# Optimization experiments

Measured on AMD Instinct MI355X. Metric: run time of the kernel, lower is better.

Reference implementation:

```python
import jax, jax.numpy as jnp
import numpy as np

DIM = 1024
HEADS = 16
DIM_HEAD = 64
INNER = HEADS * DIM_HEAD  # 1024
SCALE = DIM ** (-0.5)  # module scales by dim**-0.5 (not dim_head)


def setup_inputs() -> dict:
    key = jax.random.key(0)
    kx, kqkv, kwo, kbo = jax.random.split(key, 4)
    x = jax.random.normal(kx, (2, 2048, DIM), dtype=jnp.float32)
    W_qkv = jax.random.normal(kqkv, (DIM, 3 * INNER), dtype=jnp.float32) * (DIM ** -0.5)
    W_out = jax.random.normal(kwo, (INNER, DIM), dtype=jnp.float32) * (INNER ** -0.5)
    b_out = jax.random.normal(kbo, (DIM,), dtype=jnp.float32) * 0.01
    return {"x": x, "W_qkv": W_qkv, "W_out": W_out, "b_out": b_out}


def reference(x, W_qkv, W_out, b_out):
    b, n, _ = x.shape
    qkv = x @ W_qkv  # [b, n, 3*inner]
    q, k, v = jnp.split(qkv, 3, axis=-1)
    # [b, n, h*d] -> [b, h, n, d]
    reshape = lambda t: t.reshape(b, n, HEADS, DIM_HEAD).transpose(0, 2, 1, 3)
    q, k, v = reshape(q), reshape(k), reshape(v)
    dots = jnp.einsum('bhid,bhjd->bhij', q, k) * SCALE  # [b, h, n, n]
    attn = jax.nn.softmax(dots, axis=-1)
    out = jnp.einsum('bhij,bhjd->bhid', attn, v)  # [b, h, n, d]
    out = out.transpose(0, 2, 1, 3).reshape(b, n, INNER)
    return out @ W_out + b_out
```

## Files before the change

### kernel.cpp

```cpp
#include <hip/hip_runtime.h>

typedef __bf16 bf16x8 __attribute__((ext_vector_type(8)));
typedef __bf16 bf16x4 __attribute__((ext_vector_type(4)));
typedef __bf16 bf16x2 __attribute__((ext_vector_type(2)));
typedef float f32x4 __attribute__((ext_vector_type(4)));
typedef float f32x16 __attribute__((ext_vector_type(16)));
typedef int i32x4 __attribute__((ext_vector_type(4)));
typedef unsigned int u32x2 __attribute__((ext_vector_type(2)));

__device__ __forceinline__ void async16(void* lds, const void* g) {
  __builtin_amdgcn_global_load_lds(
      (__attribute__((address_space(1))) unsigned int*)(g),
      (__attribute__((address_space(3))) unsigned int*)(lds), 16, 0, 0);
}

__device__ __forceinline__ unsigned int pack2(float a, float b) {
  bf16x2 t;
  t[0] = (__bf16)a;
  t[1] = (__bf16)b;
  return __builtin_bit_cast(unsigned int, t);
}

__device__ __forceinline__ void plswap(unsigned int& d, unsigned int& s) {
#if __has_builtin(__builtin_amdgcn_permlane32_swap)
  u32x2 r = __builtin_amdgcn_permlane32_swap(d, s, false, false);
  d = r[0];
  s = r[1];
#else
  asm("v_permlane32_swap_b32 %0, %1" : "+v"(d), "+v"(s));
#endif
}

__device__ __forceinline__ int detect_block(const unsigned short* win, int* cnt_sh) {
  if (threadIdx.x == 0) *cnt_sh = 0;
  __syncthreads();
  int c = 0;
#pragma unroll
  for (int j = 0; j < 8; j++) {
    const unsigned short u = win[threadIdx.x * 8 + j];
    if (((u >> 7) & 0xFF) >= 0xC0) c++;
  }
  if (c) atomicAdd(cnt_sh, c);
  __syncthreads();
  return (*cnt_sh >= 64) ? 1 : 0;
}

__global__ __launch_bounds__(256) void prep(
    const void* __restrict__ x, const void* __restrict__ Wqkv,
    const void* __restrict__ Wout, __bf16* __restrict__ xb,
    __bf16* __restrict__ WqkvT, __bf16* __restrict__ WoutT,
    int* __restrict__ flagp)
{
  __shared__ __bf16 tile[64 * 65];
  __shared__ int cnt;
  const int bx = blockIdx.x;
  const int t = threadIdx.x;

  if (bx < 2048) {
    const long base = (long)bx * 2048;
    const int f = detect_block((const unsigned short*)x + base, &cnt);
    if (bx == 0 && t == 0) *flagp = f;
    const long i = base + t * 8;
    if (f) {
      const float* s = (const float*)x;
#pragma unroll
      for (int j = 0; j < 8; j++) xb[i + j] = (__bf16)s[i + j];
    } else {
      *(bf16x8*)&xb[i] = *(const bf16x8*)((const __bf16*)x + i);
    }
    return;
  }

  const void* in;  __bf16* out;  int R = 1024, C, tcx, tr;
  if (bx < 2816) {
    const int idx = bx - 2048;
    in = Wqkv; out = WqkvT; C = 3072; tcx = (idx % 48) * 64; tr = (idx / 48) * 64;
  } else {
    const int idx = bx - 2816;
    in = Wout; out = WoutT; C = 1024; tcx = (idx % 16) * 64; tr = (idx / 16) * 64;
  }
  const int f = detect_block((const unsigned short*)in + (long)tr * C + tcx, &cnt);
#pragma unroll
  for (int i = 0; i < 16; i++) {
    const int idx = t + 256 * i;
    const int r = idx >> 6, c = idx & 63;
    const long g = (long)(tr + r) * C + tcx + c;
    tile[r * 65 + c] = f ? (__bf16)((const float*)in)[g] : ((const __bf16*)in)[g];
  }
  __syncthreads();
#pragma unroll
  for (int i = 0; i < 16; i++) {
    const int idx = t + 256 * i;
    const int r = idx >> 6, c = idx & 63;
    out[(long)(tcx + r) * R + tr + c] = tile[c * 65 + r];
  }
}

__global__ __launch_bounds__(256, 3) void gemm_qkv(
    const __bf16* __restrict__ A, const __bf16* __restrict__ Bt,
    __bf16* __restrict__ Cqk, __bf16* __restrict__ Vt)
{
  __shared__ __bf16 smem[17408];
  const int t = threadIdx.x;
  const int l = t & 63;
  const int w = t >> 6;
  const int wr = w >> 1, wc = w & 1;
  const long m0 = (long)blockIdx.x * 128;
  const long n0 = (long)blockIdx.y * 128;
  const int K = 1024;

  const int srow = w * 16 + (l >> 2);
  const int skof = (l & 3) * 8;
  const __bf16* gA = A + (m0 + srow) * (long)K + skof;
  const __bf16* gB = Bt + (n0 + srow) * (long)K + skof;
  const int Ao[2] = {0, 8192}, Bo[2] = {4096, 12288};
  const int lof = w * 512 + l * 8;

  async16(smem + Ao[0] + lof,        gA);
  async16(smem + Ao[0] + 2048 + lof, gA + 64 * (long)K);
  async16(smem + Bo[0] + lof,        gB);
  async16(smem + Bo[0] + 2048 + lof, gB + 64 * (long)K);
  gA += 32; gB += 32;
  __syncthreads();

  f32x4 acc[4][4] = {};

  for (int it = 0; it < 32; it++) {
    if (it < 31) {
      const int nb = (it + 1) & 1;
      async16(smem + Ao[nb] + lof,        gA);
      async16(smem + Ao[nb] + 2048 + lof, gA + 64 * (long)K);
      async16(smem + Bo[nb] + lof,        gB);
      async16(smem + Bo[nb] + 2048 + lof, gB + 64 * (long)K);
      gA += 32; gB += 32;
    }
    const __bf16* As = smem + Ao[it & 1];
    const __bf16* Bs = smem + Bo[it & 1];
    bf16x8 af[4], bfr[4];
#pragma unroll
    for (int mi = 0; mi < 4; mi++)
      af[mi] = *(const bf16x8*)&As[(wr * 64 + mi * 16 + (l & 15)) * 32 + (l >> 4) * 8];
#pragma unroll
    for (int ni = 0; ni < 4; ni++)
      bfr[ni] = *(const bf16x8*)&Bs[(wc * 64 + ni * 16 + (l & 15)) * 32 + (l >> 4) * 8];
#pragma unroll
    for (int mi = 0; mi < 4; mi++)
#pragma unroll
      for (int ni = 0; ni < 4; ni++)
        acc[mi][ni] = __builtin_amdgcn_mfma_f32_16x16x32_bf16(af[mi], bfr[ni], acc[mi][ni], 0, 0, 0);
    __syncthreads();
  }

  if (n0 < 2048) {
#pragma unroll
    for (int mi = 0; mi < 4; mi++)
#pragma unroll
      for (int ni = 0; ni < 4; ni++) {
        const long col = n0 + wc * 64 + ni * 16 + (l & 15);
#pragma unroll
        for (int r = 0; r < 4; r++) {
          const long row = m0 + wr * 64 + mi * 16 + (l >> 4) * 4 + r;
          Cqk[row * 2048 + col] = (__bf16)acc[mi][ni][r];
        }
      }
  } else {
#pragma unroll
    for (int mi = 0; mi < 4; mi++)
#pragma unroll
      for (int ni = 0; ni < 4; ni++) {
        const int c = wc * 64 + ni * 16 + (l & 15);
        const int r = wr * 64 + mi * 16 + (l >> 4) * 4;
        bf16x4 pk;
#pragma unroll
        for (int k = 0; k < 4; k++) pk[k] = (__bf16)acc[mi][ni][k];
        *(bf16x4*)&smem[c * 136 + r] = pk;
      }
    __syncthreads();
    const int b = (int)(m0 >> 11);
    const int nbase = (int)(m0 & 2047);
#pragma unroll
    for (int i = 0; i < 8; i++) {
      const int c = (t >> 4) + i * 16;
      const int r8 = (t & 15) * 8;
      const bf16x8 v = *(const bf16x8*)&smem[c * 136 + r8];
      const int vcol = (int)(n0 - 2048) + c;
      *(bf16x8*)&Vt[((long)(b * 16 + (vcol >> 6)) * 64 + (vcol & 63)) * 2048 + nbase + r8] = v;
    }
  }
}

__global__ __launch_bounds__(256, 2) void gemm_out(
    const __bf16* __restrict__ A, const __bf16* __restrict__ Bt,
    const void* __restrict__ bias_raw, void* __restrict__ C,
    const int* __restrict__ flagp)
{
  __shared__ __bf16 smem[12288];
  const int t = threadIdx.x;
  const int l = t & 63;
  const int w = t >> 6;
  const int wr = w >> 1, wc = w & 1;
  const long m0 = (long)blockIdx.x * 128;
  const long n0 = (long)blockIdx.y * 64;
  const int of = *flagp;
  const int K = 1024;

  const int srow = w * 16 + (l >> 2);
  const int skof = (l & 3) * 8;
  const __bf16* gA = A + (m0 + srow) * (long)K + skof;
  const __bf16* gB = Bt + (n0 + srow) * (long)K + skof;
  const int Ao[2] = {0, 6144}, Bo[2] = {4096, 10240};
  const int lof = w * 512 + l * 8;

  async16(smem + Ao[0] + lof,        gA);
  async16(smem + Ao[0] + 2048 + lof, gA + 64 * (long)K);
  async16(smem + Bo[0] + lof,        gB);
  gA += 32; gB += 32;
  __syncthreads();

  f32x4 acc[4][2] = {};

  for (int it = 0; it < 32; it++) {
    if (it < 31) {
      const int nb = (it + 1) & 1;
      async16(smem + Ao[nb] + lof,        gA);
      async16(smem + Ao[nb] + 2048 + lof, gA + 64 * (long)K);
      async16(smem + Bo[nb] + lof,        gB);
      gA += 32; gB += 32;
    }
    const __bf16* As = smem + Ao[it & 1];
    const __bf16* Bs = smem + Bo[it & 1];
    bf16x8 af[4], bfr[2];
#pragma unroll
    for (int mi = 0; mi < 4; mi++)
      af[mi] = *(const bf16x8*)&As[(wr * 64 + mi * 16 + (l & 15)) * 32 + (l >> 4) * 8];
#pragma unroll
    for (int ni = 0; ni < 2; ni++)
      bfr[ni] = *(const bf16x8*)&Bs[(wc * 32 + ni * 16 + (l & 15)) * 32 + (l >> 4) * 8];
#pragma unroll
    for (int mi = 0; mi < 4; mi++)
#pragma unroll
      for (int ni = 0; ni < 2; ni++)
        acc[mi][ni] = __builtin_amdgcn_mfma_f32_16x16x32_bf16(af[mi], bfr[ni], acc[mi][ni], 0, 0, 0);
    __syncthreads();
  }

#pragma unroll
  for (int mi = 0; mi < 4; mi++)
#pragma unroll
    for (int ni = 0; ni < 2; ni++) {
      const long col = n0 + wc * 32 + ni * 16 + (l & 15);
      const float bv = of ? ((const float*)bias_raw)[col]
                          : (float)((const __bf16*)bias_raw)[col];
#pragma unroll
      for (int r = 0; r < 4; r++) {
        const long row = m0 + wr * 64 + mi * 16 + (l >> 4) * 4 + r;
        const float val = acc[mi][ni][r] + bv;
        const long off = row * 1024 + col;
        if (of) ((float*)C)[off] = val;
        else    ((__bf16*)C)[off] = (__bf16)val;
      }
    }
}

#define EXP2_SCALE 0.045084439f

__global__ __launch_bounds__(256, 4) void attn_kernel(
    const __bf16* __restrict__ qk, const __bf16* __restrict__ Vt,
    __bf16* __restrict__ O)
{
  __shared__ __bf16 smem[16384];
  const int t = threadIdx.x;
  const int l = t & 63;
  const int w = t >> 6;
  const int wi = w & 1, wj = w >> 1;
  const int hl = l >> 5;
  const int i7 = l & 7;
  const int L = blockIdx.y * 32 + blockIdx.x;
  const int bh = (L & 7) * 4 + ((L >> 3) & 3);
  const int qt = L >> 5;
  const int b = bh >> 4, head = bh & 15;
  const long q_row0 = (long)b * 2048 + qt * 64;

  const int srow = w * 8 + (l >> 3);
  const int sdof = ((l & 7) ^ (l >> 3)) * 8;
  const int lof = w * 512 + l * 8;

  const __bf16* gK = qk + ((long)b * 2048 + srow) * 2048 + 1024 + head * 64 + sdof;
  const __bf16* gV = Vt + ((long)bh * 64 + srow) * 2048 + sdof;
  async16(smem + lof,        gK);
  async16(smem + 2048 + lof, gK + 32 * 2048);
  async16(smem + 4096 + lof, gV);
  async16(smem + 6144 + lof, gV + 32 * 2048);
  gK += (long)64 * 2048;
  gV += 64;

  bf16x8 qf[4];
  {
    const __bf16* gQ = qk + (q_row0 + wi * 32 + (l & 31)) * 2048 + head * 64 + hl * 8;
#pragma unroll
    for (int kc = 0; kc < 4; kc++)
      qf[kc] = *(const bf16x8*)(gQ + kc * 16);
  }

  f32x16 accA = {0,0,0,0,0,0,0,0,0,0,0,0,0,0,0,0};
  f32x16 accB = {0,0,0,0,0,0,0,0,0,0,0,0,0,0,0,0};
  float l_i = 0.0f;

  bf16x8 pa0 = {}, pa1 = {};
  bf16x8 pvA0 = {}, pvA1 = {}, pvB0 = {}, pvB1 = {};

  const int krow = (wj * 32 + (l & 31)) * 64;
  const int vg = wj * 4;

  for (int it = 0; it < 32; it++) {
    __syncthreads();
    const __bf16* Ks = smem + (it & 1) * 8192;
    const __bf16* Vs = Ks + 4096;

    bf16x8 ak[4];
#pragma unroll
    for (int kc = 0; kc < 4; kc++)
      ak[kc] = *(const bf16x8*)&Ks[krow + (((kc * 2 + hl) ^ i7) * 8)];

    if (it < 31) {
      const int nb = ((it + 1) & 1) * 8192;
      async16(smem + nb + lof,        gK);
      async16(smem + nb + 2048 + lof, gK + 32 * 2048);
      async16(smem + nb + 4096 + lof, gV);
      async16(smem + nb + 6144 + lof, gV + 32 * 2048);
      gK += (long)64 * 2048;
      gV += 64;
    }

    __builtin_amdgcn_s_setprio(1);
    if (it > 0) {
      accA = __builtin_amdgcn_mfma_f32_32x32x16_bf16(pa0, pvA0, accA, 0, 0, 0);
      accB = __builtin_amdgcn_mfma_f32_32x32x16_bf16(pa0, pvB0, accB, 0, 0, 0);
      accA = __builtin_amdgcn_mfma_f32_32x32x16_bf16(pa1, pvA1, accA, 0, 0, 0);
      accB = __builtin_amdgcn_mfma_f32_32x32x16_bf16(pa1, pvB1, accB, 0, 0, 0);
    }
    f32x16 st = {0,0,0,0,0,0,0,0,0,0,0,0,0,0,0,0};
#pragma unroll
    for (int kc = 0; kc < 4; kc++)
      st = __builtin_amdgcn_mfma_f32_32x32x16_bf16(ak[kc], qf[kc], st, 0, 0, 0);
    __builtin_amdgcn_s_setprio(0);

    pvA0 = *(const bf16x8*)&Vs[((l & 31)) * 64      + (((vg + hl) ^ i7) * 8)];
    pvB0 = *(const bf16x8*)&Vs[(32 + (l & 31)) * 64 + (((vg + hl) ^ i7) * 8)];
    pvA1 = *(const bf16x8*)&Vs[((l & 31)) * 64      + (((vg + 2 + hl) ^ i7) * 8)];
    pvB1 = *(const bf16x8*)&Vs[(32 + (l & 31)) * 64 + (((vg + 2 + hl) ^ i7) * 8)];

    float rs = 0.0f;
#pragma unroll
    for (int r = 0; r < 16; r++) {
      const float p = exp2f(st[r] * EXP2_SCALE);
      st[r] = p;
      rs += p;
    }
    l_i += rs;

    unsigned int a0 = pack2(st[0],  st[1]),  b0 = pack2(st[4],  st[5]);
    unsigned int c0 = pack2(st[2],  st[3]),  d0 = pack2(st[6],  st[7]);
    unsigned int a1 = pack2(st[8],  st[9]),  b1 = pack2(st[12], st[13]);
    unsigned int c1 = pack2(st[10], st[11]), d1 = pack2(st[14], st[15]);
    plswap(a0, b0);
    plswap(c0, d0);
    plswap(a1, b1);
    plswap(c1, d1);
    const i32x4 f0 = {(int)a0, (int)c0, (int)b0, (int)d0};
    const i32x4 f1 = {(int)a1, (int)c1, (int)b1, (int)d1};
    pa0 = __builtin_bit_cast(bf16x8, f0);
    pa1 = __builtin_bit_cast(bf16x8, f1);
  }

  accA = __builtin_amdgcn_mfma_f32_32x32x16_bf16(pa0, pvA0, accA, 0, 0, 0);
  accB = __builtin_amdgcn_mfma_f32_32x32x16_bf16(pa0, pvB0, accB, 0, 0, 0);
  accA = __builtin_amdgcn_mfma_f32_32x32x16_bf16(pa1, pvA1, accA, 0, 0, 0);
  accB = __builtin_amdgcn_mfma_f32_32x32x16_bf16(pa1, pvB1, accB, 0, 0, 0);

  {
    unsigned int a = __builtin_bit_cast(unsigned int, l_i), bswp = a;
    plswap(a, bswp);
    l_i = __builtin_bit_cast(float, a) + __builtin_bit_cast(float, bswp);
  }

  __syncthreads();
  float* xbf = (float*)smem;
  float* lb  = (float*)(smem + 8192);
#pragma unroll
  for (int r = 0; r < 16; r++)
    xbf[w * 1024 + r * 64 + l] = wj ? accA[r] : accB[r];
  if (l < 32) lb[w * 32 + l] = l_i;
  __syncthreads();
  const int pw = 2 * (1 - wj) + wi;
#pragma unroll
  for (int r = 0; r < 16; r++) {
    const int iloc = (r & 3) + 8 * (r >> 2) + 4 * hl;
    const float lt = lb[wi * 32 + iloc] + lb[(wi + 2) * 32 + iloc];
    const float own = wj ? accB[r] : accA[r];
    const float o = own + xbf[pw * 1024 + r * 64 + l];
    const long row = q_row0 + wi * 32 + iloc;
    const long col = (long)head * 64 + wj * 32 + (l & 31);
    O[row * 1024 + col] = (__bf16)(o / lt);
  }
}

extern "C" void kernel_launch(void* const* d_in, const int* in_sizes, int n_in,
                              void* d_out, int out_size, void* d_ws, size_t ws_size,
                              hipStream_t stream) {
  const void* x    = d_in[0];
  const void* Wqkv = d_in[1];
  const void* Wout = d_in[2];
  const void* bout = d_in[3];

  char* ws = (char*)d_ws;
  int*    flagp = (int*)ws;
  __bf16* xb    = (__bf16*)(ws + 4096);
  __bf16* Obuf  = xb;
  __bf16* WqkvT = (__bf16*)(ws + 4096 +  8388608);
  __bf16* WoutT = (__bf16*)(ws + 4096 + 14680064);
  __bf16* qkbuf = (__bf16*)(ws + 4096 + 16777216);
  __bf16* VtBuf = (__bf16*)(ws + 4096 + 33554432);

  hipLaunchKernelGGL(prep, dim3(3072), dim3(256), 0, stream,
                     x, Wqkv, Wout, xb, WqkvT, WoutT, flagp);
  hipLaunchKernelGGL(gemm_qkv, dim3(32, 24), dim3(256), 0, stream,
                     xb, WqkvT, qkbuf, VtBuf);
  hipLaunchKernelGGL(attn_kernel, dim3(32, 32), dim3(256), 0, stream,
                     qkbuf, VtBuf, Obuf);
  hipLaunchKernelGGL(gemm_out, dim3(32, 16), dim3(256), 0, stream,
                     Obuf, WoutT, bout, d_out, flagp);
}
```

Baseline: 200.1 us.

## Swizzle GEMM block order and streamline attention softmax exp path

```diff
diff --git a/kernel.cpp b/kernel.cpp
--- a/kernel.cpp
+++ b/kernel.cpp
@@ -19,6 +19,14 @@
   t[0] = (__bf16)a;
   t[1] = (__bf16)b;
   return __builtin_bit_cast(unsigned int, t);
+}
+
+__device__ __forceinline__ float fexp2(float x) {
+#if __has_builtin(__builtin_amdgcn_exp2f)
+  return __builtin_amdgcn_exp2f(x);
+#else
+  return exp2f(x);
+#endif
 }
 
 __device__ __forceinline__ void plswap(unsigned int& d, unsigned int& s) {
@@ -105,8 +113,10 @@
   const int l = t & 63;
   const int w = t >> 6;
   const int wr = w >> 1, wc = w & 1;
-  const long m0 = (long)blockIdx.x * 128;
-  const long n0 = (long)blockIdx.y * 128;
+  const int lid = blockIdx.y * 32 + blockIdx.x;
+  const int s = (lid & 7) * 96 + (lid >> 3);
+  const long m0 = (long)(s & 31) * 128;
+  const long n0 = (long)(s >> 5) * 128;
   const int K = 1024;
 
   const int srow = w * 16 + (l >> 2);
@@ -199,8 +209,10 @@
   const int l = t & 63;
   const int w = t >> 6;
   const int wr = w >> 1, wc = w & 1;
-  const long m0 = (long)blockIdx.x * 128;
-  const long n0 = (long)blockIdx.y * 64;
+  const int lid = blockIdx.y * 32 + blockIdx.x;
+  const int s = (lid & 7) * 64 + (lid >> 3);
+  const long m0 = (long)(s & 31) * 128;
+  const long n0 = (long)(s >> 5) * 64;
   const int of = *flagp;
   const int K = 1024;
 
@@ -304,6 +316,7 @@
 
   f32x16 accA = {0,0,0,0,0,0,0,0,0,0,0,0,0,0,0,0};
   f32x16 accB = {0,0,0,0,0,0,0,0,0,0,0,0,0,0,0,0};
+  const f32x16 fz = {0,0,0,0,0,0,0,0,0,0,0,0,0,0,0,0};
   float l_i = 0.0f;
 
   bf16x8 pa0 = {}, pa1 = {};
@@ -339,9 +352,9 @@
       accA = __builtin_amdgcn_mfma_f32_32x32x16_bf16(pa1, pvA1, accA, 0, 0, 0);
       accB = __builtin_amdgcn_mfma_f32_32x32x16_bf16(pa1, pvB1, accB, 0, 0, 0);
     }
-    f32x16 st = {0,0,0,0,0,0,0,0,0,0,0,0,0,0,0,0};
-#pragma unroll
-    for (int kc = 0; kc < 4; kc++)
+    f32x16 st = __builtin_amdgcn_mfma_f32_32x32x16_bf16(ak[0], qf[0], fz, 0, 0, 0);
+#pragma unroll
+    for (int kc = 1; kc < 4; kc++)
       st = __builtin_amdgcn_mfma_f32_32x32x16_bf16(ak[kc], qf[kc], st, 0, 0, 0);
     __builtin_amdgcn_s_setprio(0);
 
@@ -350,14 +363,17 @@
     pvA1 = *(const bf16x8*)&Vs[((l & 31)) * 64      + (((vg + 2 + hl) ^ i7) * 8)];
     pvB1 = *(const bf16x8*)&Vs[(32 + (l & 31)) * 64 + (((vg + 2 + hl) ^ i7) * 8)];
 
-    float rs = 0.0f;
-#pragma unroll
-    for (int r = 0; r < 16; r++) {
-      const float p = exp2f(st[r] * EXP2_SCALE);
-      st[r] = p;
-      rs += p;
-    }
-    l_i += rs;
+    float rs0 = 0.0f, rs1 = 0.0f;
+#pragma unroll
+    for (int r = 0; r < 16; r += 2) {
+      const float p0 = fexp2(st[r] * EXP2_SCALE);
+      const float p1 = fexp2(st[r + 1] * EXP2_SCALE);
+      st[r] = p0;
+      st[r + 1] = p1;
+      rs0 += p0;
+      rs1 += p1;
+    }
+    l_i += rs0 + rs1;
 
     unsigned int a0 = pack2(st[0],  st[1]),  b0 = pack2(st[4],  st[5]);
     unsigned int c0 = pack2(st[2],  st[3]),  d0 = pack2(st[6],  st[7]);
```

After: 192.3 us. 3.9% less time.
